# Kernel tuning notes

Measured on AMD Instinct MI355X. Metric: run time of the kernel, lower is better.

The kernel has to match this reference:

```python
import jax, jax.numpy as jnp
import numpy as np

B, L, D = 4, 512, 768
NUM_SPANS = 4096
MAX_WIDTH = 8
DFF = 4 * D


def setup_inputs() -> dict:
    key = jax.random.key(0)
    k_h, k_s, k_w, k1, k2 = jax.random.split(key, 5)
    h = jax.random.normal(k_h, (B, L, D), dtype=jnp.float32)
    starts = jax.random.randint(k_s, (B, NUM_SPANS), 0, L)
    widths = jax.random.randint(k_w, (B, NUM_SPANS), 1, MAX_WIDTH + 1)
    ends = jnp.minimum(starts + widths - 1, L - 1)
    span_idx = jnp.stack([starts, ends], axis=-1).astype(jnp.int64 if jax.config.jax_enable_x64 else jnp.int32)
    W1 = jax.random.normal(k1, (D, DFF), dtype=jnp.float32) * (1.0 / np.sqrt(D))
    b1 = jnp.zeros((DFF,), dtype=jnp.float32)
    W2 = jax.random.normal(k2, (DFF, D), dtype=jnp.float32) * (1.0 / np.sqrt(DFF))
    b2 = jnp.zeros((D,), dtype=jnp.float32)
    return {"h": h, "span_idx": span_idx, "W1": W1, "b1": b1, "W2": W2, "b2": b2,
            "max_width": MAX_WIDTH}


def reference(h, span_idx, W1, b1, W2, b2, max_width):
    # h: [B, L, D]; span_idx: [B, S, 2] (start, end inclusive)
    Bv, Lv, Dv = h.shape
    starts = span_idx[:, :, 0]                       # [B, S]
    lengths = span_idx[:, :, 1] - starts + 1         # [B, S]
    offsets = jnp.arange(max_width)                  # static bound on span length
    positions = starts[:, :, None] + offsets[None, None, :]      # [B, S, W]
    mask = offsets[None, None, :] < lengths[:, :, None]          # [B, S, W]
    positions = jnp.clip(positions * mask, 0, Lv - 1)
    # indexed gather-reduce (no [B,S,L,D] broadcast): [B, S, W, D]
    gathered = h[jnp.arange(Bv)[:, None, None], positions]
    summed = jnp.sum(gathered * mask[..., None].astype(h.dtype), axis=2)  # [B, S, D]
    span_reps = summed / lengths[..., None].astype(h.dtype)
    # projection: Linear -> ReLU -> (Dropout: identity at eval) -> Linear
    hmid = jax.nn.relu(jnp.einsum('bsd,df->bsf', span_reps, W1) + b1)
    out = jnp.einsum('bsf,fd->bsd', hmid, W2) + b2
    return out
```

## Files before the change

### kernel.cpp

```cpp
#include <hip/hip_runtime.h>
#include <stdint.h>

#define B_DIM 4
#define L_DIM 512
#define D_DIM 768
#define S_DIM 4096
#define DFF_DIM 3072
#define M_DIM (B_DIM * S_DIM)

typedef unsigned short ushort_t;
typedef __attribute__((ext_vector_type(8))) short short8;
typedef __attribute__((ext_vector_type(4))) float floatx4;

__device__ __forceinline__ ushort_t f2bf(float x) {
  unsigned int u = __float_as_uint(x);
  u += 0x7FFFu + ((u >> 16) & 1u);
  return (ushort_t)(u >> 16);
}

__device__ __forceinline__ void load_lds16(const ushort_t* g, ushort_t* lds) {
  __builtin_amdgcn_global_load_lds(
      (const __attribute__((address_space(1))) unsigned int*)g,
      (__attribute__((address_space(3))) unsigned int*)lds, 16, 0, 0);
}

#define BARRIER()                              \
  do {                                         \
    __builtin_amdgcn_sched_barrier(0);         \
    __builtin_amdgcn_s_barrier();              \
    __builtin_amdgcn_sched_barrier(0);         \
  } while (0)

#define WAIT_LGKM0()                           \
  do {                                         \
    asm volatile("s_waitcnt lgkmcnt(0)");      \
    __builtin_amdgcn_sched_barrier(0);         \
  } while (0)

#define WAIT_VM(n)                             \
  do {                                         \
    asm volatile("s_waitcnt vmcnt(" #n ")");   \
    __builtin_amdgcn_sched_barrier(0);         \
  } while (0)

__device__ __forceinline__ void transpose_body(const float* __restrict__ in,
                                               ushort_t* __restrict__ out,
                                               int K, int N, int kb, int nb) {
  __shared__ float tile[32][33];
  const int k0 = kb * 32;
  const int n0 = nb * 32;
  const int tx = threadIdx.x & 31;
  const int ty = threadIdx.x >> 5;
#pragma unroll
  for (int r = 0; r < 32; r += 8)
    tile[ty + r][tx] = in[(long)(k0 + ty + r) * N + n0 + tx];
  __syncthreads();
#pragma unroll
  for (int r = 0; r < 32; r += 8)
    out[(long)(n0 + ty + r) * K + k0 + tx] = f2bf(tile[tx][ty + r]);
}

__device__ __forceinline__ void span_body(const float* __restrict__ h,
                                          const int* __restrict__ span_idx,
                                          ushort_t* __restrict__ A, int blk) {
  const int wave = threadIdx.x >> 6;
  const int lane = threadIdx.x & 63;
  const int span = blk * 4 + wave;
  const int b = span >> 12;
  const int start = span_idx[span * 2 + 0];
  const int end   = span_idx[span * 2 + 1];
  const float inv = 1.0f / (float)(end - start + 1);
  const float* hb = h + ((long)b * L_DIM + start) * D_DIM + lane;
  float a[12];
#pragma unroll
  for (int c = 0; c < 12; ++c) a[c] = 0.0f;
  for (int p = start; p <= end; ++p) {
#pragma unroll
    for (int c = 0; c < 12; ++c) a[c] += hb[c * 64];
    hb += D_DIM;
  }
  ushort_t* o = A + (long)span * D_DIM + lane;
#pragma unroll
  for (int c = 0; c < 12; ++c) o[c * 64] = f2bf(a[c] * inv);
}

__global__ __launch_bounds__(256)
void prep(const float* __restrict__ W1, ushort_t* __restrict__ W1T,
          const float* __restrict__ W2, ushort_t* __restrict__ W2T,
          const float* __restrict__ h, const int* __restrict__ span_idx,
          ushort_t* __restrict__ A) {
  const int blk = blockIdx.x;
  if (blk < 2304) {
    transpose_body(W1, W1T, D_DIM, DFF_DIM, blk % 24, blk / 24);
  } else if (blk < 4608) {
    const int b = blk - 2304;
    transpose_body(W2, W2T, DFF_DIM, D_DIM, b % 96, b / 96);
  } else {
    span_body(h, span_idx, A, blk - 4608);
  }
}

template <int MODE>
__global__ __launch_bounds__(512, 2)
void gemm256(const ushort_t* __restrict__ A, const ushort_t* __restrict__ Bt,
             const float* __restrict__ bias, void* __restrict__ Cv,
             int M, int N, int K) {
  __shared__ ushort_t As[2][256 * 64];
  __shared__ ushort_t Bs[2][256 * 64];

  const int tid  = threadIdx.x;
  const int lane = tid & 63;
  const int l16  = lane & 15;
  const int quad = lane >> 4;
  const int wave = tid >> 6;
  const int wr   = wave >> 2;
  const int wc   = wave & 3;

  const int bm = blockIdx.x;
  const int bn = blockIdx.y;

  const int srow   = tid >> 3;
  const int schunk = (tid & 7) ^ (srow & 7);
  const ushort_t* gA = A  + (long)(bm * 256 + srow) * K + schunk * 8;
  const ushort_t* gB = Bt + (long)(bn * 256 + srow) * K + schunk * 8;
  const long rK64 = (long)K * 64;
  ushort_t* lA = &As[0][0] + tid * 8;
  ushort_t* lB = &Bs[0][0] + tid * 8;

  auto STAGE_LO = [&](int buf, int kt) {
    const ushort_t* ga = gA + (long)kt * 64;
    const ushort_t* gb = gB + (long)kt * 64;
    ushort_t* la = lA + buf * (256 * 64);
    ushort_t* lb = lB + buf * (256 * 64);
    load_lds16(ga,        la);
    load_lds16(ga + rK64, la + 4096);
    load_lds16(gb,        lb);
    load_lds16(gb + rK64, lb + 4096);
  };
  auto STAGE_HI = [&](int buf, int kt) {
    const ushort_t* ga = gA + (long)kt * 64 + 2 * rK64;
    const ushort_t* gb = gB + (long)kt * 64 + 2 * rK64;
    ushort_t* la = lA + buf * (256 * 64);
    ushort_t* lb = lB + buf * (256 * 64);
    load_lds16(ga,        la + 8192);
    load_lds16(ga + rK64, la + 12288);
    load_lds16(gb,        lb + 8192);
    load_lds16(gb + rK64, lb + 12288);
  };

  const int arow0 = (wr * 128 + l16) * 64;
  const int brow0 = (wc * 64 + l16) * 64;
  const int cx0 = ((quad)     ^ (l16 & 7)) << 3;
  const int cx1 = ((quad + 4) ^ (l16 & 7)) << 3;

  floatx4 acc[8][4];
#pragma unroll
  for (int i = 0; i < 8; ++i)
#pragma unroll
    for (int j = 0; j < 4; ++j) acc[i][j] = (floatx4)0.0f;

  const int nk = K >> 6;

  STAGE_LO(0, 0);
  STAGE_HI(0, 0);
  if (nk > 1) {
    STAGE_LO(1, 1);
    WAIT_VM(4);
  } else {
    WAIT_VM(0);
  }
  BARRIER();

  short8 af[4][2], bf[4][2];

  for (int k = 0; k < nk; ++k) {
    const int cur = k & 1;
    const int nxt = cur ^ 1;
    const ushort_t* Ac = &As[cur][0];
    const ushort_t* Bc = &Bs[cur][0];

    if (k + 1 < nk) STAGE_HI(nxt, k + 1);
#pragma unroll
    for (int i = 0; i < 4; ++i) {
      af[i][0] = *(const short8*)(Ac + arow0 + i * 1024 + cx0);
      af[i][1] = *(const short8*)(Ac + arow0 + i * 1024 + cx1);
    }
#pragma unroll
    for (int j = 0; j < 2; ++j) {
      bf[j][0] = *(const short8*)(Bc + brow0 + j * 1024 + cx0);
      bf[j][1] = *(const short8*)(Bc + brow0 + j * 1024 + cx1);
    }
    BARRIER();
    WAIT_LGKM0();
    __builtin_amdgcn_s_setprio(1);
#pragma unroll
    for (int i = 0; i < 4; ++i)
#pragma unroll
      for (int j = 0; j < 2; ++j) {
        acc[i][j] = __builtin_amdgcn_mfma_f32_16x16x32_bf16(af[i][0], bf[j][0], acc[i][j], 0, 0, 0);
        acc[i][j] = __builtin_amdgcn_mfma_f32_16x16x32_bf16(af[i][1], bf[j][1], acc[i][j], 0, 0, 0);
      }
    __builtin_amdgcn_s_setprio(0);
    BARRIER();

#pragma unroll
    for (int j = 0; j < 2; ++j) {
      bf[2 + j][0] = *(const short8*)(Bc + brow0 + (2 + j) * 1024 + cx0);
      bf[2 + j][1] = *(const short8*)(Bc + brow0 + (2 + j) * 1024 + cx1);
    }
    BARRIER();
    WAIT_LGKM0();
    __builtin_amdgcn_s_setprio(1);
#pragma unroll
    for (int i = 0; i < 4; ++i)
#pragma unroll
      for (int j = 0; j < 2; ++j) {
        acc[i][2 + j] = __builtin_amdgcn_mfma_f32_16x16x32_bf16(af[i][0], bf[2 + j][0], acc[i][2 + j], 0, 0, 0);
        acc[i][2 + j] = __builtin_amdgcn_mfma_f32_16x16x32_bf16(af[i][1], bf[2 + j][1], acc[i][2 + j], 0, 0, 0);
      }
    __builtin_amdgcn_s_setprio(0);
    BARRIER();

#pragma unroll
    for (int i = 0; i < 4; ++i) {
      af[i][0] = *(const short8*)(Ac + arow0 + (4 + i) * 1024 + cx0);
      af[i][1] = *(const short8*)(Ac + arow0 + (4 + i) * 1024 + cx1);
    }
    BARRIER();
    WAIT_LGKM0();
    __builtin_amdgcn_s_setprio(1);
#pragma unroll
    for (int i = 0; i < 4; ++i)
#pragma unroll
      for (int j = 0; j < 2; ++j) {
        acc[4 + i][2 + j] = __builtin_amdgcn_mfma_f32_16x16x32_bf16(af[i][0], bf[2 + j][0], acc[4 + i][2 + j], 0, 0, 0);
        acc[4 + i][2 + j] = __builtin_amdgcn_mfma_f32_16x16x32_bf16(af[i][1], bf[2 + j][1], acc[4 + i][2 + j], 0, 0, 0);
      }
    __builtin_amdgcn_s_setprio(0);
    BARRIER();

    if (k + 2 < nk) {
      STAGE_LO(cur, k + 2);
      __builtin_amdgcn_s_setprio(1);
#pragma unroll
      for (int i = 0; i < 4; ++i)
#pragma unroll
        for (int j = 0; j < 2; ++j) {
          acc[4 + i][j] = __builtin_amdgcn_mfma_f32_16x16x32_bf16(af[i][0], bf[j][0], acc[4 + i][j], 0, 0, 0);
          acc[4 + i][j] = __builtin_amdgcn_mfma_f32_16x16x32_bf16(af[i][1], bf[j][1], acc[4 + i][j], 0, 0, 0);
        }
      __builtin_amdgcn_s_setprio(0);
      WAIT_VM(4);
    } else {
      __builtin_amdgcn_s_setprio(1);
#pragma unroll
      for (int i = 0; i < 4; ++i)
#pragma unroll
        for (int j = 0; j < 2; ++j) {
          acc[4 + i][j] = __builtin_amdgcn_mfma_f32_16x16x32_bf16(af[i][0], bf[j][0], acc[4 + i][j], 0, 0, 0);
          acc[4 + i][j] = __builtin_amdgcn_mfma_f32_16x16x32_bf16(af[i][1], bf[j][1], acc[4 + i][j], 0, 0, 0);
        }
      __builtin_amdgcn_s_setprio(0);
      WAIT_VM(0);
    }
    BARRIER();
  }

  const long rowbase = (long)bm * 256 + wr * 128 + quad * 4;
  const int  colbase = bn * 256 + wc * 64 + l16;
#pragma unroll
  for (int j = 0; j < 4; ++j) {
    const int col = colbase + j * 16;
    const float bv = bias[col];
#pragma unroll
    for (int i = 0; i < 8; ++i) {
      const long row0 = rowbase + i * 16;
#pragma unroll
      for (int r = 0; r < 4; ++r) {
        float v = acc[i][j][r] + bv;
        if (MODE == 0) {
          v = v > 0.0f ? v : 0.0f;
          ((ushort_t*)Cv)[(row0 + r) * N + col] = f2bf(v);
        } else {
          ((float*)Cv)[(row0 + r) * N + col] = v;
        }
      }
    }
  }
}

extern "C" void kernel_launch(void* const* d_in, const int* in_sizes, int n_in,
                              void* d_out, int out_size, void* d_ws, size_t ws_size,
                              hipStream_t stream) {
  const float* h        = (const float*)d_in[0];
  const int*   span_idx = (const int*)d_in[1];
  const float* W1       = (const float*)d_in[2];
  const float* b1       = (const float*)d_in[3];
  const float* W2       = (const float*)d_in[4];
  const float* b2       = (const float*)d_in[5];
  float* out = (float*)d_out;

  ushort_t* A   = (ushort_t*)d_ws;
  ushort_t* W1T = A + (size_t)M_DIM * D_DIM;
  ushort_t* W2T = W1T + (size_t)DFF_DIM * D_DIM;
  ushort_t* Hm  = W2T + (size_t)D_DIM * DFF_DIM;

  prep<<<2304 + 2304 + M_DIM / 4, 256, 0, stream>>>(W1, W1T, W2, W2T, h, span_idx, A);

  gemm256<0><<<dim3(M_DIM / 256, DFF_DIM / 256), 512, 0, stream>>>(
      A, W1T, b1, Hm, M_DIM, DFF_DIM, D_DIM);

  gemm256<1><<<dim3(M_DIM / 256, D_DIM / 256), 512, 0, stream>>>(
      Hm, W2T, b2, out, M_DIM, D_DIM, DFF_DIM);
}
```

Before: 309.2 us.

## Vectorize span gather and remap GEMM tiles to XCD-local blocks

The span-averaging loop now loads float4 vectors and writes packed 4×bf16 stores, replacing 12 scalar loads and stores per lane. Both GEMMs switch to a 1D grid where each block's id is remapped so that consecutive ids round-robin across the 8 XCDs. Each XCD then gets a contiguous group of 8 M-tiles for every N-tile, so A tiles are reused from that XCD's L2. The mapping hardcodes M/256=64 tiles, which holds for this shape.

```diff
diff --git a/kernel.cpp b/kernel.cpp
--- a/kernel.cpp
+++ b/kernel.cpp
@@ -10,6 +10,7 @@
 
 typedef unsigned short ushort_t;
 typedef __attribute__((ext_vector_type(8))) short short8;
+typedef __attribute__((ext_vector_type(4))) short short4v;
 typedef __attribute__((ext_vector_type(4))) float floatx4;
 
 __device__ __forceinline__ ushort_t f2bf(float x) {
@@ -70,18 +71,24 @@
   const int start = span_idx[span * 2 + 0];
   const int end   = span_idx[span * 2 + 1];
   const float inv = 1.0f / (float)(end - start + 1);
-  const float* hb = h + ((long)b * L_DIM + start) * D_DIM + lane;
-  float a[12];
-#pragma unroll
-  for (int c = 0; c < 12; ++c) a[c] = 0.0f;
+  const floatx4* hb =
+      (const floatx4*)(h + ((long)b * L_DIM + start) * D_DIM) + lane;
+  floatx4 a[3];
+#pragma unroll
+  for (int c = 0; c < 3; ++c) a[c] = (floatx4)0.0f;
   for (int p = start; p <= end; ++p) {
 #pragma unroll
-    for (int c = 0; c < 12; ++c) a[c] += hb[c * 64];
-    hb += D_DIM;
-  }
-  ushort_t* o = A + (long)span * D_DIM + lane;
-#pragma unroll
-  for (int c = 0; c < 12; ++c) o[c * 64] = f2bf(a[c] * inv);
+    for (int c = 0; c < 3; ++c) a[c] += hb[c * 64];
+    hb += 192;
+  }
+  short4v* o = (short4v*)(A + (long)span * D_DIM) + lane;
+#pragma unroll
+  for (int c = 0; c < 3; ++c) {
+    short4v s;
+#pragma unroll
+    for (int e = 0; e < 4; ++e) s[e] = (short)f2bf(a[c][e] * inv);
+    o[c * 64] = s;
+  }
 }
 
 __global__ __launch_bounds__(256)
@@ -116,8 +123,11 @@
   const int wr   = wave >> 2;
   const int wc   = wave & 3;
 
-  const int bm = blockIdx.x;
-  const int bn = blockIdx.y;
+  const int id  = blockIdx.x;
+  const int xcd = id & 7;
+  const int l   = id >> 3;
+  const int bm  = xcd * 8 + (l & 7);
+  const int bn  = l >> 3;
 
   const int srow   = tid >> 3;
   const int schunk = (tid & 7) ^ (srow & 7);
@@ -307,9 +317,9 @@
 
   prep<<<2304 + 2304 + M_DIM / 4, 256, 0, stream>>>(W1, W1T, W2, W2T, h, span_idx, A);
 
-  gemm256<0><<<dim3(M_DIM / 256, DFF_DIM / 256), 512, 0, stream>>>(
+  gemm256<0><<<dim3((M_DIM / 256) * (DFF_DIM / 256)), 512, 0, stream>>>(
       A, W1T, b1, Hm, M_DIM, DFF_DIM, D_DIM);
 
-  gemm256<1><<<dim3(M_DIM / 256, D_DIM / 256), 512, 0, stream>>>(
+  gemm256<1><<<dim3((M_DIM / 256) * (D_DIM / 256)), 512, 0, stream>>>(
       Hm, W2T, b2, out, M_DIM, D_DIM, DFF_DIM);
 }
```

Measured after the change: 309.1 us. About the same (-0.0%).
